# Kernel tuning notes

Hardware: AMD Instinct MI355X
Metric: run time of the kernel (lower is better)

Reference implementation:

```python
import jax, jax.numpy as jnp
import numpy as np

VOCAB = 3149
T_MAX = 256
C = 128      # n_emb
H = 8        # n_heads
D = C // H   # head_size = 16
L = 6        # n blocks
FF = 4 * C
EPS = 1e-5


def _layernorm(x, g, b):
    mu = jnp.mean(x, axis=-1, keepdims=True)
    var = jnp.mean((x - mu) ** 2, axis=-1, keepdims=True)
    return (x - mu) / jnp.sqrt(var + EPS) * g + b


def setup_inputs() -> dict:
    key = jax.random.key(0)
    ks = jax.random.split(key, 24)
    s = 0.02
    inp = {
        "tokens": jax.random.randint(ks[0], (64, 256), 0, VOCAB),
        "tok_emb": jax.random.normal(ks[1], (VOCAB, C), jnp.float32) * s,
        "pos_emb": jax.random.normal(ks[2], (T_MAX, C), jnp.float32) * s,
        "Wq": jax.random.normal(ks[3], (L, H, C, D), jnp.float32) * s,
        "Wk": jax.random.normal(ks[4], (L, H, C, D), jnp.float32) * s,
        "Wv": jax.random.normal(ks[5], (L, H, C, D), jnp.float32) * s,
        "Wproj": jax.random.normal(ks[6], (L, C, C), jnp.float32) * s,
        "bproj": jnp.zeros((L, C), jnp.float32),
        "ln1_g": jnp.ones((L, C), jnp.float32),
        "ln1_b": jnp.zeros((L, C), jnp.float32),
        "ln2_g": jnp.ones((L, C), jnp.float32),
        "ln2_b": jnp.zeros((L, C), jnp.float32),
        "W1": jax.random.normal(ks[7], (L, C, FF), jnp.float32) * s,
        "b1": jnp.zeros((L, FF), jnp.float32),
        "W2": jax.random.normal(ks[8], (L, FF, C), jnp.float32) * s,
        "b2": jnp.zeros((L, C), jnp.float32),
        "lnf_g": jnp.ones((C,), jnp.float32),
        "lnf_b": jnp.zeros((C,), jnp.float32),
        "Wlm": jax.random.normal(ks[9], (C, VOCAB), jnp.float32) * s,
        "blm": jnp.zeros((VOCAB,), jnp.float32),
    }
    return inp


def reference(tokens, tok_emb, pos_emb, Wq, Wk, Wv, Wproj, bproj,
              ln1_g, ln1_b, ln2_g, ln2_b, W1, b1, W2, b2,
              lnf_g, lnf_b, Wlm, blm):
    B, T = tokens.shape
    x = tok_emb[tokens] + pos_emb[:T][None, :, :]  # (B,T,C)
    # NOTE: original code scales scores by C**-0.5 with C = n_emb (128), not head_size.
    scale = jnp.asarray(C, x.dtype) ** -0.5
    causal = jnp.tril(jnp.ones((T, T), bool))
    neg_inf = jnp.asarray(-jnp.inf, x.dtype)
    for l in range(L):
        xn = _layernorm(x, ln1_g[l], ln1_b[l])
        q = jnp.einsum('btc,hcd->bhtd', xn, Wq[l])
        k = jnp.einsum('btc,hcd->bhtd', xn, Wk[l])
        v = jnp.einsum('btc,hcd->bhtd', xn, Wv[l])
        wei = jnp.einsum('bhtd,bhsd->bhts', q, k) * scale
        wei = jnp.where(causal[None, None], wei, neg_inf)
        wei = jax.nn.softmax(wei, axis=-1)
        attn = jnp.einsum('bhts,bhsd->bhtd', wei, v)
        attn = attn.transpose(0, 2, 1, 3).reshape(B, T, C)  # concat heads
        x = x + jnp.einsum('btc,cf->btf', attn, Wproj[l]) + bproj[l]
        xn2 = _layernorm(x, ln2_g[l], ln2_b[l])
        h = jax.nn.relu(jnp.einsum('btc,cf->btf', xn2, W1[l]) + b1[l])
        x = x + jnp.einsum('btf,fc->btc', h, W2[l]) + b2[l]
    x = _layernorm(x, lnf_g, lnf_b)
    logits = jnp.einsum('btc,cv->btv', x, Wlm) + blm
    return logits
```

## Files before the change

kernel.cpp:

```cpp
#include <hip/hip_runtime.h>
#include <hip/hip_bf16.h>
#include <math.h>

#define BT   16384
#define CDIM 128
#define TSEQ 256
#define NBAT 64
#define NH   8
#define HD   16
#define NL   6
#define FFD  512
#define NV   3149

typedef __bf16 bfv8 __attribute__((ext_vector_type(8)));
typedef float  fv4  __attribute__((ext_vector_type(4)));
typedef unsigned short u16;
typedef unsigned int   u32;
typedef u16 u16v8 __attribute__((ext_vector_type(8)));

__device__ __forceinline__ u16 f2b(float f) {
  u32 u = __builtin_bit_cast(u32, f);
  u += 0x7FFFu + ((u >> 16) & 1u);
  return (u16)(u >> 16);
}
__device__ __forceinline__ float b2f(u16 h) {
  return __builtin_bit_cast(float, (u32)h << 16);
}
__device__ __forceinline__ u32 cvtpk(float lo, float hi) {
  u32 r;
  asm("v_cvt_pk_bf16_f32 %0, %1, %2" : "=v"(r) : "v"(lo), "v"(hi));
  return r;
}

__global__ __launch_bounds__(256) void embed_kernel(
    const int* __restrict__ tokens, const float* __restrict__ tok_emb,
    const float* __restrict__ pos_emb, float* __restrict__ x) {
  int i4 = blockIdx.x * 256 + threadIdx.x;
  if (i4 >= BT * CDIM / 4) return;
  int i  = i4 * 4;
  int c  = i & (CDIM - 1);
  int bt = i >> 7;
  int t  = bt & (TSEQ - 1);
  int tok = tokens[bt];
  float4 te = *(const float4*)(tok_emb + (size_t)tok * CDIM + c);
  float4 pe = *(const float4*)(pos_emb + (size_t)t * CDIM + c);
  float4 r;
  r.x = te.x + pe.x; r.y = te.y + pe.y; r.z = te.z + pe.z; r.w = te.w + pe.w;
  *(float4*)(x + i) = r;
}

__global__ __launch_bounds__(256) void packqkv_bf16(
    const float* __restrict__ Wq, const float* __restrict__ Wk,
    const float* __restrict__ Wv, u16* __restrict__ dst) {
  int idx = blockIdx.x * 256 + threadIdx.x;
  if (idx >= NL * 384 * CDIM) return;
  int c = idx & 127;
  int j = (idx >> 7) % 384;
  int l = idx / (384 * CDIM);
  int sel = j >> 7;
  int jj  = j & 127;
  int h   = jj >> 4;
  int d   = jj & 15;
  const float* W = (sel == 0) ? Wq : (sel == 1) ? Wk : Wv;
  dst[idx] = f2b(W[(((size_t)l * NH + h) * CDIM + c) * HD + d]);
}

__global__ __launch_bounds__(256) void transpose_cast(
    const float* __restrict__ src, u16* __restrict__ dst, int R, int C, int L) {
  int idx = blockIdx.x * 256 + threadIdx.x;
  if (idx >= L * R * C) return;
  int r = idx % R;
  int c = (idx / R) % C;
  int l = idx / (R * C);
  dst[idx] = f2b(src[((size_t)l * R + r) * C + c]);
}

__global__ __launch_bounds__(256) void ln_kernel(
    const float* __restrict__ x, const float* __restrict__ g,
    const float* __restrict__ b, u16* __restrict__ out) {
  int wid  = blockIdx.x * 4 + (threadIdx.x >> 6);
  int lane = threadIdx.x & 63;
  const float2 v = ((const float2*)(x + (size_t)wid * CDIM))[lane];
  float s = v.x + v.y;
  #pragma unroll
  for (int m = 1; m < 64; m <<= 1) s += __shfl_xor(s, m);
  float mu = s * (1.f / CDIM);
  float dx = v.x - mu, dy = v.y - mu;
  float s2 = dx * dx + dy * dy;
  #pragma unroll
  for (int m = 1; m < 64; m <<= 1) s2 += __shfl_xor(s2, m);
  float rstd = rsqrtf(s2 * (1.f / CDIM) + 1e-5f);
  float2 gg = ((const float2*)g)[lane];
  float2 bb = ((const float2*)b)[lane];
  u32 pack = (u32)f2b(dx * rstd * gg.x + bb.x) |
             ((u32)f2b(dy * rstd * gg.y + bb.y) << 16);
  ((u32*)(out + (size_t)wid * CDIM))[lane] = pack;
}

template<int OMODE, bool BIAS, bool RELU, int BN>
__global__ __launch_bounds__(256) void gemm_mfma(
    const u16* __restrict__ A, const u16* __restrict__ Btp,
    const float* __restrict__ bias, void* __restrict__ Cout,
    int M, int N, int K) {
  constexpr int BM = 128, BK = 32, PAD = 40;
  constexpr int NF = BN / 32;
  __shared__ u16 As[BM][PAD];
  __shared__ u16 Bs[BN][PAD];
  const int tid  = threadIdx.x;
  const int lane = tid & 63;
  const int wv   = tid >> 6;
  const int wm   = wv & 1;
  const int wn   = wv >> 1;
  const int m0 = blockIdx.y * BM;
  const int n0 = blockIdx.x * BN;
  const int srow = tid >> 2;
  const int sk8  = (tid & 3) * 8;
  const int fr = lane & 15;
  const int fk = (lane >> 4) * 8;

  fv4 acc[4][NF];
  #pragma unroll
  for (int i = 0; i < 4; i++)
    #pragma unroll
    for (int j = 0; j < NF; j++) acc[i][j] = (fv4){0.f, 0.f, 0.f, 0.f};

  for (int k0 = 0; k0 < K; k0 += BK) {
    #pragma unroll
    for (int p = 0; p < 2; p++) {
      int r = srow + p * 64;
      *(uint4*)&As[r][sk8] = *(const uint4*)(A + (size_t)(m0 + r) * K + k0 + sk8);
    }
    #pragma unroll
    for (int p = 0; p < BN / 64; p++) {
      int r = srow + p * 64;
      int n = n0 + r;
      uint4 v = make_uint4(0u, 0u, 0u, 0u);
      if (n < N) v = *(const uint4*)(Btp + (size_t)n * K + k0 + sk8);
      *(uint4*)&Bs[r][sk8] = v;
    }
    __syncthreads();
    bfv8 a[4], b[NF];
    #pragma unroll
    for (int i = 0; i < 4; i++)
      a[i] = *(const bfv8*)&As[wm * 64 + i * 16 + fr][fk];
    #pragma unroll
    for (int j = 0; j < NF; j++)
      b[j] = *(const bfv8*)&Bs[wn * (BN / 2) + j * 16 + fr][fk];
    #pragma unroll
    for (int i = 0; i < 4; i++)
      #pragma unroll
      for (int j = 0; j < NF; j++)
        acc[i][j] = __builtin_amdgcn_mfma_f32_16x16x32_bf16(a[i], b[j], acc[i][j], 0, 0, 0);
    __syncthreads();
  }

  const int row0 = m0 + wm * 64;
  const int col0 = n0 + wn * (BN / 2);
  const int lr   = (lane >> 4) * 4;
  #pragma unroll
  for (int j = 0; j < NF; j++) {
    int col = col0 + j * 16 + fr;
    if (col >= N) continue;
    float bz = BIAS ? bias[col] : 0.f;
    #pragma unroll
    for (int i = 0; i < 4; i++) {
      #pragma unroll
      for (int q = 0; q < 4; q++) {
        int row = row0 + i * 16 + lr + q;
        float v = acc[i][j][q] + bz;
        if (RELU) v = fmaxf(v, 0.f);
        if (OMODE == 0)      ((u16*)Cout)[(size_t)row * N + col] = f2b(v);
        else if (OMODE == 1) ((float*)Cout)[(size_t)row * N + col] = v;
        else                 ((float*)Cout)[(size_t)row * N + col] += v;
      }
    }
  }
}

__global__ __launch_bounds__(256) void attn_mfma(
    const u16* __restrict__ qkv, u16* __restrict__ out) {
  const float scale = 0.08838834764831843f;
  __shared__ u16 Qs[TSEQ][40];
  __shared__ u16 Ks[TSEQ][40];
  __shared__ u16 Vt[HD][280];
  const int bh = blockIdx.x;
  const int h = bh & (NH - 1);
  const int b = bh >> 3;
  const int tid = threadIdx.x;

  #pragma unroll
  for (int p = 0; p < 2; p++) {
    int idx = tid + p * 256;
    int r  = idx >> 1;
    int c8 = (idx & 1) * 8;
    const u16* base = qkv + (size_t)(b * TSEQ + r) * 384 + h * HD + c8;
    uint4 q = *(const uint4*)(base);
    uint4 k = *(const uint4*)(base + CDIM);
    u16v8 v = *(const u16v8*)(base + 2 * CDIM);
    *(uint4*)&Qs[r][c8] = q;
    *(uint4*)&Ks[r][c8] = k;
    if (c8 == 0) {
      uint4 z = make_uint4(0u, 0u, 0u, 0u);
      *(uint4*)&Qs[r][16] = z; *(uint4*)&Qs[r][24] = z;
      *(uint4*)&Ks[r][16] = z; *(uint4*)&Ks[r][24] = z;
    }
    #pragma unroll
    for (int i = 0; i < 8; i++) Vt[c8 + i][r] = v[i];
  }
  __syncthreads();

  const int wv   = tid >> 6;
  const int lane = tid & 63;
  const int fr = lane & 15;
  const int g  = lane >> 4;
  const int fk = g * 8;

  const int qts[4] = {wv, 7 - wv, 8 + wv, 15 - wv};

  #pragma unroll
  for (int qi = 0; qi < 4; qi++) {
    const int qt = qts[qi];
    bfv8 qf = *(const bfv8*)&Qs[qt * 16 + fr][fk];

    fv4 sf[16];
    #pragma unroll
    for (int st = 0; st < 16; st++) {
      if (st <= qt) {
        bfv8 kf = *(const bfv8*)&Ks[st * 16 + fr][fk];
        fv4 z = (fv4){0.f, 0.f, 0.f, 0.f};
        sf[st] = __builtin_amdgcn_mfma_f32_16x16x32_bf16(kf, qf, z, 0, 0, 0);
      }
    }

    float mx = -3.4e38f;
    #pragma unroll
    for (int st = 0; st < 16; st++) {
      if (st <= qt) {
        #pragma unroll
        for (int r = 0; r < 4; r++) {
          float v = sf[st][r] * scale;
          if (st == qt && (4 * g + r) > fr) v = -3.4e38f;
          sf[st][r] = v;
          mx = fmaxf(mx, v);
        }
      }
    }
    mx = fmaxf(mx, __shfl_xor(mx, 16));
    mx = fmaxf(mx, __shfl_xor(mx, 32));

    float sum = 0.f;
    #pragma unroll
    for (int st = 0; st < 16; st++) {
      if (st <= qt) {
        #pragma unroll
        for (int r = 0; r < 4; r++) {
          float p = __expf(sf[st][r] - mx);
          sf[st][r] = p;
          sum += p;
        }
      }
    }
    sum += __shfl_xor(sum, 16);
    sum += __shfl_xor(sum, 32);
    const float inv = 1.f / sum;

    fv4 accO = (fv4){0.f, 0.f, 0.f, 0.f};
    #pragma unroll
    for (int ks = 0; ks < 8; ks++) {
      if (2 * ks <= qt) {
        u32 E0 = cvtpk(sf[2 * ks][0], sf[2 * ks][1]);
        u32 E1 = cvtpk(sf[2 * ks][2], sf[2 * ks][3]);
        u32 O0 = 0u, O1 = 0u;
        if (2 * ks + 1 <= qt) {
          O0 = cvtpk(sf[2 * ks + 1][0], sf[2 * ks + 1][1]);
          O1 = cvtpk(sf[2 * ks + 1][2], sf[2 * ks + 1][3]);
        }
        u32 w[4];
        #pragma unroll
        for (int ww = 0; ww < 4; ww++) {
          int src = (2 * (g & 1) + (ww >> 1)) * 16 + fr;
          u32 tE = __shfl((ww & 1) ? E1 : E0, src);
          u32 tO = __shfl((ww & 1) ? O1 : O0, src);
          w[ww] = (g >= 2) ? tO : tE;
        }
        uint4 uw = make_uint4(w[0], w[1], w[2], w[3]);
        bfv8 pf = __builtin_bit_cast(bfv8, uw);
        bfv8 vf = *(const bfv8*)&Vt[fr][ks * 32 + fk];
        accO = __builtin_amdgcn_mfma_f32_16x16x32_bf16(vf, pf, accO, 0, 0, 0);
      }
    }

    int q_glob = qt * 16 + fr;
    u32 lo = cvtpk(accO[0] * inv, accO[1] * inv);
    u32 hi = cvtpk(accO[2] * inv, accO[3] * inv);
    uint2 st2 = make_uint2(lo, hi);
    *(uint2*)(out + (size_t)(b * TSEQ + q_glob) * CDIM + h * HD + 4 * g) = st2;
  }
}

extern "C" void kernel_launch(void* const* d_in, const int* in_sizes, int n_in,
                              void* d_out, int out_size, void* d_ws, size_t ws_size,
                              hipStream_t stream) {
  const int*   tokens  = (const int*)  d_in[0];
  const float* tok_emb = (const float*)d_in[1];
  const float* pos_emb = (const float*)d_in[2];
  const float* Wq      = (const float*)d_in[3];
  const float* Wk      = (const float*)d_in[4];
  const float* Wv      = (const float*)d_in[5];
  const float* Wproj   = (const float*)d_in[6];
  const float* bproj   = (const float*)d_in[7];
  const float* ln1_g   = (const float*)d_in[8];
  const float* ln1_b   = (const float*)d_in[9];
  const float* ln2_g   = (const float*)d_in[10];
  const float* ln2_b   = (const float*)d_in[11];
  const float* W1      = (const float*)d_in[12];
  const float* b1      = (const float*)d_in[13];
  const float* W2      = (const float*)d_in[14];
  const float* b2      = (const float*)d_in[15];
  const float* lnf_g   = (const float*)d_in[16];
  const float* lnf_b   = (const float*)d_in[17];
  const float* Wlm     = (const float*)d_in[18];
  const float* blm     = (const float*)d_in[19];
  float* out = (float*)d_out;

  char* W = (char*)d_ws;
  float* x    = (float*)(W);
  u16*   xn   = (u16*)  (W + 8388608);
  u16*   qkvb = (u16*)  (W + 12582912);
  u16*   att  = (u16*)  (W + 25165824);
  u16*   hbuf = (u16*)  (W + 29360128);
  u16*   wqkv = (u16*)  (W + 46137344);
  u16*   wpj  = (u16*)  (W + 46727168);
  u16*   w1t  = (u16*)  (W + 46923776);
  u16*   w2t  = (u16*)  (W + 47710208);
  u16*   wlmt = (u16*)  (W + 48496640);

  packqkv_bf16<<<(NL * 384 * CDIM + 255) / 256, 256, 0, stream>>>(Wq, Wk, Wv, wqkv);
  transpose_cast<<<(NL * CDIM * CDIM + 255) / 256, 256, 0, stream>>>(Wproj, wpj, CDIM, CDIM, NL);
  transpose_cast<<<(NL * CDIM * FFD + 255) / 256, 256, 0, stream>>>(W1, w1t, CDIM, FFD, NL);
  transpose_cast<<<(NL * FFD * CDIM + 255) / 256, 256, 0, stream>>>(W2, w2t, FFD, CDIM, NL);
  transpose_cast<<<(CDIM * NV + 255) / 256, 256, 0, stream>>>(Wlm, wlmt, CDIM, NV, 1);
  embed_kernel<<<(BT * CDIM / 4 + 255) / 256, 256, 0, stream>>>(tokens, tok_emb, pos_emb, x);

  for (int l = 0; l < NL; l++) {
    ln_kernel<<<BT / 4, 256, 0, stream>>>(x, ln1_g + l * CDIM, ln1_b + l * CDIM, xn);
    gemm_mfma<0, false, false, 128><<<dim3(3, BT / 128), 256, 0, stream>>>(
        xn, wqkv + (size_t)l * 384 * CDIM, nullptr, qkvb, BT, 384, CDIM);
    attn_mfma<<<NBAT * NH, 256, 0, stream>>>(qkvb, att);
    gemm_mfma<2, true, false, 64><<<dim3(2, BT / 128), 256, 0, stream>>>(
        att, wpj + (size_t)l * CDIM * CDIM, bproj + l * CDIM, x, BT, CDIM, CDIM);
    ln_kernel<<<BT / 4, 256, 0, stream>>>(x, ln2_g + l * CDIM, ln2_b + l * CDIM, xn);
    gemm_mfma<0, true, true, 128><<<dim3(4, BT / 128), 256, 0, stream>>>(
        xn, w1t + (size_t)l * FFD * CDIM, b1 + l * FFD, hbuf, BT, FFD, CDIM);
    gemm_mfma<2, true, false, 64><<<dim3(2, BT / 128), 256, 0, stream>>>(
        hbuf, w2t + (size_t)l * CDIM * FFD, b2 + l * CDIM, x, BT, CDIM, FFD);
  }
  ln_kernel<<<BT / 4, 256, 0, stream>>>(x, lnf_g, lnf_b, xn);
  gemm_mfma<1, true, false, 128><<<dim3((NV + 127) / 128, BT / 128), 256, 0, stream>>>(
      xn, wlmt, blm, out, BT, NV, CDIM);
}
```

Measured before the change: 856.9 us.

## Fuse layernorm into GEMMs, split attention queries, use 16x16x16 MFMA

```diff
diff --git a/kernel.cpp b/kernel.cpp
--- a/kernel.cpp
+++ b/kernel.cpp
@@ -14,6 +14,7 @@
 
 typedef __bf16 bfv8 __attribute__((ext_vector_type(8)));
 typedef float  fv4  __attribute__((ext_vector_type(4)));
+typedef short  s4   __attribute__((ext_vector_type(4)));
 typedef unsigned short u16;
 typedef unsigned int   u32;
 typedef u16 u16v8 __attribute__((ext_vector_type(8)));
@@ -23,13 +24,20 @@
   u += 0x7FFFu + ((u >> 16) & 1u);
   return (u16)(u >> 16);
 }
-__device__ __forceinline__ float b2f(u16 h) {
-  return __builtin_bit_cast(float, (u32)h << 16);
-}
 __device__ __forceinline__ u32 cvtpk(float lo, float hi) {
   u32 r;
   asm("v_cvt_pk_bf16_f32 %0, %1, %2" : "=v"(r) : "v"(lo), "v"(hi));
   return r;
+}
+__device__ __forceinline__ fv4 mfma16(s4 a, s4 b, fv4 c) {
+#if __has_builtin(__builtin_amdgcn_mfma_f32_16x16x16bf16_1k)
+  return __builtin_amdgcn_mfma_f32_16x16x16bf16_1k(a, b, c, 0, 0, 0);
+#else
+  fv4 d;
+  asm volatile("v_mfma_f32_16x16x16_bf16 %0, %1, %2, %3"
+               : "=v"(d) : "v"(a), "v"(b), "v"(c));
+  return d;
+#endif
 }
 
 __global__ __launch_bounds__(256) void embed_kernel(
@@ -65,14 +73,23 @@
   dst[idx] = f2b(W[(((size_t)l * NH + h) * CDIM + c) * HD + d]);
 }
 
-__global__ __launch_bounds__(256) void transpose_cast(
-    const float* __restrict__ src, u16* __restrict__ dst, int R, int C, int L) {
-  int idx = blockIdx.x * 256 + threadIdx.x;
-  if (idx >= L * R * C) return;
-  int r = idx % R;
-  int c = (idx / R) % C;
-  int l = idx / (R * C);
-  dst[idx] = f2b(src[((size_t)l * R + r) * C + c]);
+__global__ __launch_bounds__(256) void transpose_cast_t(
+    const float* __restrict__ src, u16* __restrict__ dst, int R, int C) {
+  __shared__ float tile[32][33];
+  int l  = blockIdx.z;
+  int r0 = blockIdx.y * 32, c0 = blockIdx.x * 32;
+  int tr = threadIdx.x >> 5, tc = threadIdx.x & 31;
+  #pragma unroll
+  for (int p = 0; p < 4; p++) {
+    int r = r0 + tr + p * 8, c = c0 + tc;
+    if (r < R && c < C) tile[tr + p * 8][tc] = src[((size_t)l * R + r) * C + c];
+  }
+  __syncthreads();
+  #pragma unroll
+  for (int p = 0; p < 4; p++) {
+    int c = c0 + tr + p * 8, r = r0 + tc;
+    if (r < R && c < C) dst[((size_t)l * C + c) * R + r] = f2b(tile[tc][tr + p * 8]);
+  }
 }
 
 __global__ __launch_bounds__(256) void ln_kernel(
@@ -177,15 +194,108 @@
   }
 }
 
+template<bool BIAS, bool RELU>
+__global__ __launch_bounds__(256) void gemm_ln_mfma(
+    const float* __restrict__ X, const u16* __restrict__ Btp,
+    const float* __restrict__ lng, const float* __restrict__ lnb,
+    const float* __restrict__ bias, u16* __restrict__ Cout,
+    int M, int N) {
+  constexpr int BM = 128, BN = 128, BK = 32;
+  __shared__ u16 As[BM][136];
+  __shared__ u16 Bs[BN][40];
+  const int tid  = threadIdx.x;
+  const int lane = tid & 63;
+  const int wv   = tid >> 6;
+  const int wm   = wv & 1;
+  const int wn   = wv >> 1;
+  const int m0 = blockIdx.y * BM;
+  const int n0 = blockIdx.x * BN;
+  const int fr = lane & 15;
+  const int fk = (lane >> 4) * 8;
+
+  {
+    const int l32  = lane & 31;
+    const int rsel = lane >> 5;
+    float4 gg = *(const float4*)(lng + l32 * 4);
+    float4 bb = *(const float4*)(lnb + l32 * 4);
+    #pragma unroll 4
+    for (int it = 0; it < 16; it++) {
+      int r = wv * 32 + it * 2 + rsel;
+      float4 v = *(const float4*)(X + (size_t)(m0 + r) * 128 + l32 * 4);
+      float s = (v.x + v.y) + (v.z + v.w);
+      #pragma unroll
+      for (int m = 1; m < 32; m <<= 1) s += __shfl_xor(s, m);
+      float mu = s * (1.f / 128.f);
+      float dx = v.x - mu, dy = v.y - mu, dz = v.z - mu, dw = v.w - mu;
+      float s2 = (dx * dx + dy * dy) + (dz * dz + dw * dw);
+      #pragma unroll
+      for (int m = 1; m < 32; m <<= 1) s2 += __shfl_xor(s2, m);
+      float rstd = rsqrtf(s2 * (1.f / 128.f) + 1e-5f);
+      u32 p0 = cvtpk(dx * rstd * gg.x + bb.x, dy * rstd * gg.y + bb.y);
+      u32 p1 = cvtpk(dz * rstd * gg.z + bb.z, dw * rstd * gg.w + bb.w);
+      *(uint2*)&As[r][l32 * 4] = make_uint2(p0, p1);
+    }
+  }
+
+  fv4 acc[4][4];
+  #pragma unroll
+  for (int i = 0; i < 4; i++)
+    #pragma unroll
+    for (int j = 0; j < 4; j++) acc[i][j] = (fv4){0.f, 0.f, 0.f, 0.f};
+
+  for (int k0 = 0; k0 < 128; k0 += BK) {
+    #pragma unroll
+    for (int p = 0; p < 2; p++) {
+      int ch = tid + p * 256;
+      int row = ch >> 2, c8 = (ch & 3) * 8;
+      *(uint4*)&Bs[row][c8] = *(const uint4*)(Btp + (size_t)(n0 + row) * 128 + k0 + c8);
+    }
+    __syncthreads();
+    bfv8 a[4], b[4];
+    #pragma unroll
+    for (int i = 0; i < 4; i++)
+      a[i] = *(const bfv8*)&As[wm * 64 + i * 16 + fr][k0 + fk];
+    #pragma unroll
+    for (int j = 0; j < 4; j++)
+      b[j] = *(const bfv8*)&Bs[wn * 64 + j * 16 + fr][fk];
+    #pragma unroll
+    for (int i = 0; i < 4; i++)
+      #pragma unroll
+      for (int j = 0; j < 4; j++)
+        acc[i][j] = __builtin_amdgcn_mfma_f32_16x16x32_bf16(a[i], b[j], acc[i][j], 0, 0, 0);
+    __syncthreads();
+  }
+
+  const int row0 = m0 + wm * 64;
+  const int col0 = n0 + wn * 64;
+  const int lr   = (lane >> 4) * 4;
+  #pragma unroll
+  for (int j = 0; j < 4; j++) {
+    int col = col0 + j * 16 + fr;
+    float bz = BIAS ? bias[col] : 0.f;
+    #pragma unroll
+    for (int i = 0; i < 4; i++) {
+      #pragma unroll
+      for (int q = 0; q < 4; q++) {
+        int row = row0 + i * 16 + lr + q;
+        float v = acc[i][j][q] + bz;
+        if (RELU) v = fmaxf(v, 0.f);
+        Cout[(size_t)row * N + col] = f2b(v);
+      }
+    }
+  }
+}
+
 __global__ __launch_bounds__(256) void attn_mfma(
     const u16* __restrict__ qkv, u16* __restrict__ out) {
   const float scale = 0.08838834764831843f;
-  __shared__ u16 Qs[TSEQ][40];
-  __shared__ u16 Ks[TSEQ][40];
+  __shared__ u16 Qs[128][20];
+  __shared__ u16 Ks[TSEQ][20];
   __shared__ u16 Vt[HD][280];
-  const int bh = blockIdx.x;
-  const int h = bh & (NH - 1);
-  const int b = bh >> 3;
+  const int blk = blockIdx.x;
+  const int qh = blk & 1;
+  const int h  = (blk >> 1) & (NH - 1);
+  const int b  = blk >> 4;
   const int tid = threadIdx.x;
 
   #pragma unroll
@@ -194,18 +304,17 @@
     int r  = idx >> 1;
     int c8 = (idx & 1) * 8;
     const u16* base = qkv + (size_t)(b * TSEQ + r) * 384 + h * HD + c8;
-    uint4 q = *(const uint4*)(base);
-    uint4 k = *(const uint4*)(base + CDIM);
-    u16v8 v = *(const u16v8*)(base + 2 * CDIM);
-    *(uint4*)&Qs[r][c8] = q;
+    uint4 k  = *(const uint4*)(base + CDIM);
+    u16v8 v  = *(const u16v8*)(base + 2 * CDIM);
     *(uint4*)&Ks[r][c8] = k;
-    if (c8 == 0) {
-      uint4 z = make_uint4(0u, 0u, 0u, 0u);
-      *(uint4*)&Qs[r][16] = z; *(uint4*)&Qs[r][24] = z;
-      *(uint4*)&Ks[r][16] = z; *(uint4*)&Ks[r][24] = z;
-    }
     #pragma unroll
     for (int i = 0; i < 8; i++) Vt[c8 + i][r] = v[i];
+  }
+  {
+    int r  = tid >> 1;
+    int c8 = (tid & 1) * 8;
+    const u16* base = qkv + (size_t)(b * TSEQ + qh * 128 + r) * 384 + h * HD + c8;
+    *(uint4*)&Qs[r][c8] = *(const uint4*)(base);
   }
   __syncthreads();
 
@@ -213,22 +322,19 @@
   const int lane = tid & 63;
   const int fr = lane & 15;
   const int g  = lane >> 4;
-  const int fk = g * 8;
-
-  const int qts[4] = {wv, 7 - wv, 8 + wv, 15 - wv};
-
-  #pragma unroll
-  for (int qi = 0; qi < 4; qi++) {
-    const int qt = qts[qi];
-    bfv8 qf = *(const bfv8*)&Qs[qt * 16 + fr][fk];
+
+  #pragma unroll 1
+  for (int qi = 0; qi < 2; qi++) {
+    const int qt = qh * 8 + (qi ? (7 - wv) : wv);
+    const int qr = (qt - qh * 8) * 16 + fr;
+    s4 qf = *(const s4*)&Qs[qr][g * 4];
 
     fv4 sf[16];
     #pragma unroll
     for (int st = 0; st < 16; st++) {
       if (st <= qt) {
-        bfv8 kf = *(const bfv8*)&Ks[st * 16 + fr][fk];
-        fv4 z = (fv4){0.f, 0.f, 0.f, 0.f};
-        sf[st] = __builtin_amdgcn_mfma_f32_16x16x32_bf16(kf, qf, z, 0, 0, 0);
+        s4 kf = *(const s4*)&Ks[st * 16 + fr][g * 4];
+        sf[st] = mfma16(kf, qf, (fv4){0.f, 0.f, 0.f, 0.f});
       }
     }
 
@@ -249,15 +355,14 @@
     mx = fmaxf(mx, __shfl_xor(mx, 32));
 
     float sum = 0.f;
+    uint2 pk[16];
     #pragma unroll
     for (int st = 0; st < 16; st++) {
       if (st <= qt) {
-        #pragma unroll
-        for (int r = 0; r < 4; r++) {
-          float p = __expf(sf[st][r] - mx);
-          sf[st][r] = p;
-          sum += p;
-        }
+        float e0 = __expf(sf[st][0] - mx), e1 = __expf(sf[st][1] - mx);
+        float e2 = __expf(sf[st][2] - mx), e3 = __expf(sf[st][3] - mx);
+        sum += (e0 + e1) + (e2 + e3);
+        pk[st] = make_uint2(cvtpk(e0, e1), cvtpk(e2, e3));
       }
     }
     sum += __shfl_xor(sum, 16);
@@ -266,35 +371,19 @@
 
     fv4 accO = (fv4){0.f, 0.f, 0.f, 0.f};
     #pragma unroll
-    for (int ks = 0; ks < 8; ks++) {
-      if (2 * ks <= qt) {
-        u32 E0 = cvtpk(sf[2 * ks][0], sf[2 * ks][1]);
-        u32 E1 = cvtpk(sf[2 * ks][2], sf[2 * ks][3]);
-        u32 O0 = 0u, O1 = 0u;
-        if (2 * ks + 1 <= qt) {
-          O0 = cvtpk(sf[2 * ks + 1][0], sf[2 * ks + 1][1]);
-          O1 = cvtpk(sf[2 * ks + 1][2], sf[2 * ks + 1][3]);
-        }
-        u32 w[4];
-        #pragma unroll
-        for (int ww = 0; ww < 4; ww++) {
-          int src = (2 * (g & 1) + (ww >> 1)) * 16 + fr;
-          u32 tE = __shfl((ww & 1) ? E1 : E0, src);
-          u32 tO = __shfl((ww & 1) ? O1 : O0, src);
-          w[ww] = (g >= 2) ? tO : tE;
-        }
-        uint4 uw = make_uint4(w[0], w[1], w[2], w[3]);
-        bfv8 pf = __builtin_bit_cast(bfv8, uw);
-        bfv8 vf = *(const bfv8*)&Vt[fr][ks * 32 + fk];
-        accO = __builtin_amdgcn_mfma_f32_16x16x32_bf16(vf, pf, accO, 0, 0, 0);
-      }
-    }
-
-    int q_glob = qt * 16 + fr;
+    for (int st = 0; st < 16; st++) {
+      if (st <= qt) {
+        s4 vf = *(const s4*)&Vt[fr][st * 16 + g * 4];
+        s4 pf = __builtin_bit_cast(s4, pk[st]);
+        accO = mfma16(vf, pf, accO);
+      }
+    }
+
+    const int q_glob = qt * 16 + fr;
     u32 lo = cvtpk(accO[0] * inv, accO[1] * inv);
     u32 hi = cvtpk(accO[2] * inv, accO[3] * inv);
-    uint2 st2 = make_uint2(lo, hi);
-    *(uint2*)(out + (size_t)(b * TSEQ + q_glob) * CDIM + h * HD + 4 * g) = st2;
+    *(uint2*)(out + (size_t)(b * TSEQ + q_glob) * CDIM + h * HD + 4 * g) =
+        make_uint2(lo, hi);
   }
 }
 
@@ -336,22 +425,22 @@
   u16*   wlmt = (u16*)  (W + 48496640);
 
   packqkv_bf16<<<(NL * 384 * CDIM + 255) / 256, 256, 0, stream>>>(Wq, Wk, Wv, wqkv);
-  transpose_cast<<<(NL * CDIM * CDIM + 255) / 256, 256, 0, stream>>>(Wproj, wpj, CDIM, CDIM, NL);
-  transpose_cast<<<(NL * CDIM * FFD + 255) / 256, 256, 0, stream>>>(W1, w1t, CDIM, FFD, NL);
-  transpose_cast<<<(NL * FFD * CDIM + 255) / 256, 256, 0, stream>>>(W2, w2t, FFD, CDIM, NL);
-  transpose_cast<<<(CDIM * NV + 255) / 256, 256, 0, stream>>>(Wlm, wlmt, CDIM, NV, 1);
+  transpose_cast_t<<<dim3(4, 4, NL), 256, 0, stream>>>(Wproj, wpj, CDIM, CDIM);
+  transpose_cast_t<<<dim3(16, 4, NL), 256, 0, stream>>>(W1, w1t, CDIM, FFD);
+  transpose_cast_t<<<dim3(4, 16, NL), 256, 0, stream>>>(W2, w2t, FFD, CDIM);
+  transpose_cast_t<<<dim3((NV + 31) / 32, 4, 1), 256, 0, stream>>>(Wlm, wlmt, CDIM, NV);
   embed_kernel<<<(BT * CDIM / 4 + 255) / 256, 256, 0, stream>>>(tokens, tok_emb, pos_emb, x);
 
   for (int l = 0; l < NL; l++) {
-    ln_kernel<<<BT / 4, 256, 0, stream>>>(x, ln1_g + l * CDIM, ln1_b + l * CDIM, xn);
-    gemm_mfma<0, false, false, 128><<<dim3(3, BT / 128), 256, 0, stream>>>(
-        xn, wqkv + (size_t)l * 384 * CDIM, nullptr, qkvb, BT, 384, CDIM);
-    attn_mfma<<<NBAT * NH, 256, 0, stream>>>(qkvb, att);
+    gemm_ln_mfma<false, false><<<dim3(3, BT / 128), 256, 0, stream>>>(
+        x, wqkv + (size_t)l * 384 * CDIM, ln1_g + l * CDIM, ln1_b + l * CDIM,
+        nullptr, qkvb, BT, 384);
+    attn_mfma<<<NBAT * NH * 2, 256, 0, stream>>>(qkvb, att);
     gemm_mfma<2, true, false, 64><<<dim3(2, BT / 128), 256, 0, stream>>>(
         att, wpj + (size_t)l * CDIM * CDIM, bproj + l * CDIM, x, BT, CDIM, CDIM);
-    ln_kernel<<<BT / 4, 256, 0, stream>>>(x, ln2_g + l * CDIM, ln2_b + l * CDIM, xn);
-    gemm_mfma<0, true, true, 128><<<dim3(4, BT / 128), 256, 0, stream>>>(
-        xn, w1t + (size_t)l * FFD * CDIM, b1 + l * FFD, hbuf, BT, FFD, CDIM);
+    gemm_ln_mfma<true, true><<<dim3(4, BT / 128), 256, 0, stream>>>(
+        x, w1t + (size_t)l * FFD * CDIM, ln2_g + l * CDIM, ln2_b + l * CDIM,
+        b1 + l * FFD, hbuf, BT, FFD);
     gemm_mfma<2, true, false, 64><<<dim3(2, BT / 128), 256, 0, stream>>>(
         hbuf, w2t + (size_t)l * CDIM * FFD, b2 + l * CDIM, x, BT, CDIM, FFD);
   }
```

Measured after the change: 847.4 us. Within noise of the previous version (-1.1%).
